# Kernel optimization log

Measured on AMD Instinct MI355X. Metric: run time of the kernel, lower is better.

## Reference

```python
import jax, jax.numpy as jnp
import numpy as np

H = 2048          # hidden_size
I = 8192          # intermediate_size (shared expert)
E = 32            # num_experts
K = 4             # num_experts_per_tok
M = 1408          # moe_intermediate_size
B, S = 2, 1024


def setup_inputs() -> dict:
    key = jax.random.key(0)
    ks = jax.random.split(key, 7)
    scale = 0.02
    return {
        "hidden_states": jax.random.normal(ks[0], (B, S, H), dtype=jnp.float32),
        "gate_w": jax.random.normal(ks[1], (H, E), dtype=jnp.float32) * scale,
        "w1": jax.random.normal(ks[2], (E, H, M), dtype=jnp.float32) * scale,  # expert up-proj
        "w2": jax.random.normal(ks[3], (E, M, H), dtype=jnp.float32) * scale,  # expert down-proj
        "ws1": jax.random.normal(ks[4], (H, I), dtype=jnp.float32) * scale,    # shared up-proj
        "ws2": jax.random.normal(ks[5], (I, H), dtype=jnp.float32) * scale,    # shared down-proj
    }


def reference(hidden_states, gate_w, w1, w2, ws1, ws2):
    b, s, h = hidden_states.shape
    x = hidden_states.reshape(-1, h)                      # [T, H]

    # shared expert: Linear -> SiLU -> Linear
    shared = jax.nn.silu(x @ ws1) @ ws2                   # [T, H]

    # router: top-k logits, softmax over the k selected logits
    router_logits = x @ gate_w                            # [T, E]
    top_vals, top_idx = jax.lax.top_k(router_logits, K)   # [T, K]
    routing_weights = jax.nn.softmax(top_vals, axis=-1)   # [T, K]

    # combine weights: scatter top-k weights into dense [T, E]
    cw = (jax.nn.one_hot(top_idx, E, dtype=x.dtype)
          * routing_weights[..., None]).sum(axis=1)       # [T, E]

    # expert FFNs (dense over experts, weighted combine)
    a = jax.nn.silu(jnp.einsum('th,ehm->tem', x, w1))     # [T, E, M]
    expert_out = jnp.einsum('tem,emh,te->th', a, w2, cw)  # [T, H]

    output = (shared + expert_out).reshape(b, s, h)
    return output, router_logits.reshape(b, s, E)
```

## Files before the change

### kernel.cpp

```cpp
#include <hip/hip_runtime.h>

#define H_ 2048
#define E_ 32
#define KSEL 4
#define M_ 1408
#define I_ 8192
#define T_ 2048

typedef __bf16 bf16;
typedef bf16 bf16x8 __attribute__((ext_vector_type(8)));
typedef float f32x4 __attribute__((ext_vector_type(4)));
typedef unsigned short u16x8 __attribute__((ext_vector_type(8)));
typedef unsigned int u32x4 __attribute__((ext_vector_type(4)));

static __device__ __forceinline__ unsigned short bfb(float f) {
  return __builtin_bit_cast(unsigned short, (bf16)f);
}

static __device__ __forceinline__ void gload_lds16(const void* g, void* l) {
  __builtin_amdgcn_global_load_lds((const __attribute__((address_space(1))) void*)g,
                                   (__attribute__((address_space(3))) void*)l, 16, 0, 0);
}

static __device__ __forceinline__ float silu_f(float v) {
  return v / (1.f + __expf(-v));
}

static __device__ __forceinline__ void wave_argmax(float& v, int& vi) {
  #pragma unroll
  for (int off = 32; off >= 1; off >>= 1) {
    float ov = __shfl_xor(v, off);
    int   oi = __shfl_xor(vi, off);
    if (ov > v || (ov == v && oi < vi)) { v = ov; vi = oi; }
  }
}

__global__ __launch_bounds__(256) void prep_k(float* __restrict__ out, int* __restrict__ counts) {
  size_t i = ((size_t)blockIdx.x * 256 + threadIdx.x) * 4;
  *(float4*)(out + i) = make_float4(0.f, 0.f, 0.f, 0.f);
  if (blockIdx.x == 0 && threadIdx.x < E_) counts[threadIdx.x] = 0;
}

__global__ __launch_bounds__(256) void cvt_k(const float* __restrict__ x, unsigned short* __restrict__ xb) {
  size_t i = ((size_t)blockIdx.x * 256 + threadIdx.x) * 8;
  float4 a = *(const float4*)(x + i);
  float4 b = *(const float4*)(x + i + 4);
  u16x8 o;
  o[0]=bfb(a.x); o[1]=bfb(a.y); o[2]=bfb(a.z); o[3]=bfb(a.w);
  o[4]=bfb(b.x); o[5]=bfb(b.y); o[6]=bfb(b.z); o[7]=bfb(b.w);
  *(u16x8*)(xb + i) = o;
}

__global__ __launch_bounds__(256) void combine_k(const float* __restrict__ sc, float* __restrict__ out) {
  size_t i = ((size_t)blockIdx.x * 256 + threadIdx.x) * 4;
  int t = (int)(i >> 11);
  int h = (int)(i & 2047);
  const float* s = sc + (size_t)(t * 4) * H_ + h;
  float4 a = *(const float4*)(s);
  float4 b = *(const float4*)(s + H_);
  float4 c = *(const float4*)(s + 2 * H_);
  float4 d = *(const float4*)(s + 3 * H_);
  float4 o = *(const float4*)(out + i);
  o.x += a.x + b.x + c.x + d.x;
  o.y += a.y + b.y + c.y + d.y;
  o.z += a.z + b.z + c.z + d.z;
  o.w += a.w + b.w + c.w + d.w;
  *(float4*)(out + i) = o;
}

__global__ __launch_bounds__(64) void router_k(const float* __restrict__ x, const float* __restrict__ gw,
                                               float* __restrict__ logits, int* __restrict__ counts,
                                               int* __restrict__ tlist, float* __restrict__ wlist) {
  int t = blockIdx.x;
  int l = threadIdx.x;
  int e = l & 31;
  int half = l >> 5;
  const float* xr = x + (size_t)t * H_ + half * (H_/2);
  const float* g  = gw + (size_t)(half * (H_/2)) * E_ + e;
  float a0=0.f, a1=0.f, a2=0.f, a3=0.f;
  for (int h = 0; h < H_/2; h += 4) {
    a0 = fmaf(xr[h],   g[(size_t)h*E_],     a0);
    a1 = fmaf(xr[h+1], g[(size_t)(h+1)*E_], a1);
    a2 = fmaf(xr[h+2], g[(size_t)(h+2)*E_], a2);
    a3 = fmaf(xr[h+3], g[(size_t)(h+3)*E_], a3);
  }
  float acc = (a0+a1)+(a2+a3);
  acc += __shfl_xor(acc, 32);
  if (l < E_) logits[(size_t)t*E_ + l] = acc;

  float cur = (l < E_) ? acc : -INFINITY;
  int myidx = (l < E_) ? e : 1000;
  float tv0,tv1,tv2,tv3; int ti0,ti1,ti2,ti3;
  { float v=cur; int vi=myidx; wave_argmax(v,vi); tv0=v; ti0=vi; if (myidx==vi) cur=-INFINITY; }
  { float v=cur; int vi=myidx; wave_argmax(v,vi); tv1=v; ti1=vi; if (myidx==vi) cur=-INFINITY; }
  { float v=cur; int vi=myidx; wave_argmax(v,vi); tv2=v; ti2=vi; if (myidx==vi) cur=-INFINITY; }
  { float v=cur; int vi=myidx; wave_argmax(v,vi); tv3=v; ti3=vi; }
  float w0 = 1.f;
  float w1 = __expf(tv1 - tv0);
  float w2 = __expf(tv2 - tv0);
  float w3 = __expf(tv3 - tv0);
  float inv = 1.f / (w0+w1+w2+w3);
  if (l < KSEL) {
    float myw = ((l==0)?w0:(l==1)?w1:(l==2)?w2:w3) * inv;
    int   myi = ((l==0)?ti0:(l==1)?ti1:(l==2)?ti2:ti3);
    int pos = atomicAdd(&counts[myi], 1);
    tlist[myi*T_ + pos] = (t << 2) | l;
    wlist[myi*T_ + pos] = myw;
  }
}

template<int MODE, int KDIM, int NDIM, int ASTR, int KSPLIT>
__global__ __launch_bounds__(256) void gemm_k(
    const bf16* __restrict__ A, const float* __restrict__ Bf,
    bf16* __restrict__ Cb, float* __restrict__ Cf,
    const int* __restrict__ tlist, const float* __restrict__ wlist,
    const int* __restrict__ counts)
{
  __shared__ __align__(16) char smem[16384];
  char* As = smem;
  char* Bs = smem + 8192;
  const int tid = threadIdx.x;

  int mt, nt, e = 0, kz = 0;
  int nrows = T_;
  const int* lst = nullptr;
  const float* Bp = Bf;
  if constexpr (MODE == 2 || MODE == 3) {
    constexpr int NT = NDIM / 128;
    e  = blockIdx.x / NT;
    nt = blockIdx.x % NT;
    mt = blockIdx.y;
    nrows = counts[e];
    if (mt * 128 >= nrows) return;
    lst = tlist + e*T_;
    Bp = Bf + (size_t)e * ((size_t)KDIM * NDIM);
    if constexpr (KSPLIT > 1) kz = blockIdx.z;
  } else {
    constexpr int NWG = 16 * (NDIM / 128);
    constexpr int CPX = NWG / 8;
    int id = blockIdx.x;
    int lg = (id & 7) * CPX + (id >> 3);
    mt = lg & 15;
    nt = lg >> 4;
    if constexpr (KSPLIT > 1) kz = blockIdx.z;
  }
  const int mrow0 = mt*128, ncol0 = nt*128;

  const bf16* abase[2];
  int aoffs[2];
  #pragma unroll
  for (int hh = 0; hh < 2; ++hh) {
    int lidx = hh*256 + tid;
    int row  = lidx >> 2;
    int slog = (lidx & 3) ^ (row & 3);
    aoffs[hh] = slog * 8;
    int ri = mrow0 + row;
    if constexpr (MODE == 2) {
      int tt = (ri < nrows) ? (lst[ri] >> 2) : 0;
      abase[hh] = A + (size_t)tt * ASTR;
    } else if constexpr (MODE == 3) {
      int ar = (ri < nrows) ? lst[ri] : 0;
      abase[hh] = A + (size_t)ar * ASTR;
    } else {
      abase[hh] = A + (size_t)ri * ASTR;
    }
  }

  const int bn = tid & 127;
  const int bh = tid >> 7;
  const float* bsrc0 = Bp + (size_t)(bh * 16) * NDIM + ncol0 + bn;
  char* bdst0 = Bs + (bh*2)*2048 + bn*16;

  const int l  = tid & 63;
  const int wv = tid >> 6;
  const int wr = wv >> 1, wc = wv & 1;
  const int ss = l >> 4;

  f32x4 acc[4][4] = {};

  constexpr int ITERS = KDIM / 32 / KSPLIT;
  static_assert(ITERS % 2 == 0, "K-loop is 2-unrolled");
  const int kt0 = kz * ITERS;
  const int ktend = kt0 + ITERS;

  float vA0,vA1,vA2,vA3,vA4,vA5,vA6,vA7,vA8,vA9,vA10,vA11,vA12,vA13,vA14,vA15;
  float vB0,vB1,vB2,vB3,vB4,vB5,vB6,vB7,vB8,vB9,vB10,vB11,vB12,vB13,vB14,vB15;

#define LOADB(P, KT) do {                                            \
    const float* bs_ = bsrc0 + (size_t)((KT) * 32) * NDIM;           \
    P##0 = bs_[0];            P##1 = bs_[(size_t)1*NDIM];            \
    P##2 = bs_[(size_t)2*NDIM];  P##3 = bs_[(size_t)3*NDIM];         \
    P##4 = bs_[(size_t)4*NDIM];  P##5 = bs_[(size_t)5*NDIM];         \
    P##6 = bs_[(size_t)6*NDIM];  P##7 = bs_[(size_t)7*NDIM];         \
    P##8 = bs_[(size_t)8*NDIM];  P##9 = bs_[(size_t)9*NDIM];         \
    P##10 = bs_[(size_t)10*NDIM]; P##11 = bs_[(size_t)11*NDIM];      \
    P##12 = bs_[(size_t)12*NDIM]; P##13 = bs_[(size_t)13*NDIM];      \
    P##14 = bs_[(size_t)14*NDIM]; P##15 = bs_[(size_t)15*NDIM];      \
  } while (0)

#define WRITEB(P) do {                                               \
    u32x4 lo_, hi_;                                                  \
    lo_[0] = (unsigned)bfb(P##0)  | ((unsigned)bfb(P##1)  << 16);    \
    lo_[1] = (unsigned)bfb(P##2)  | ((unsigned)bfb(P##3)  << 16);    \
    lo_[2] = (unsigned)bfb(P##4)  | ((unsigned)bfb(P##5)  << 16);    \
    lo_[3] = (unsigned)bfb(P##6)  | ((unsigned)bfb(P##7)  << 16);    \
    hi_[0] = (unsigned)bfb(P##8)  | ((unsigned)bfb(P##9)  << 16);    \
    hi_[1] = (unsigned)bfb(P##10) | ((unsigned)bfb(P##11) << 16);    \
    hi_[2] = (unsigned)bfb(P##12) | ((unsigned)bfb(P##13) << 16);    \
    hi_[3] = (unsigned)bfb(P##14) | ((unsigned)bfb(P##15) << 16);    \
    *(u32x4*)(bdst0)        = lo_;                                   \
    *(u32x4*)(bdst0 + 2048) = hi_;                                   \
  } while (0)

#define MFMA_PHASE(KT) do {                                          \
    bf16x8 af[4], bfr[4];                                            \
    _Pragma("unroll")                                                \
    for (int mf = 0; mf < 4; ++mf) {                                 \
      int r = wr*64 + mf*16 + (l & 15);                              \
      af[mf] = *(const bf16x8*)(As + r*64 + ((ss ^ (r & 3)) << 4));  \
    }                                                                \
    _Pragma("unroll")                                                \
    for (int nf = 0; nf < 4; ++nf) {                                 \
      int c = wc*64 + nf*16 + (l & 15);                              \
      bfr[nf] = *(const bf16x8*)(Bs + ss*2048 + c*16);               \
    }                                                                \
    _Pragma("unroll")                                                \
    for (int mf = 0; mf < 4; ++mf)                                   \
      _Pragma("unroll")                                              \
      for (int nf = 0; nf < 4; ++nf)                                 \
        acc[mf][nf] = __builtin_amdgcn_mfma_f32_16x16x32_bf16(af[mf], bfr[nf], acc[mf][nf], 0, 0, 0); \
  } while (0)

#define ADMA(KT) do {                                                \
    _Pragma("unroll")                                                \
    for (int hh = 0; hh < 2; ++hh)                                   \
      gload_lds16(abase[hh] + (KT)*32 + aoffs[hh], As + (hh*256 + tid)*16); \
  } while (0)

  LOADB(vA, kt0);
  for (int kt = kt0; kt < ktend; kt += 2) {
    __syncthreads();
    ADMA(kt);
    WRITEB(vA);
    __syncthreads();
    LOADB(vB, kt + 1);
    MFMA_PHASE(kt);

    __syncthreads();
    ADMA(kt + 1);
    WRITEB(vB);
    __syncthreads();
    if (kt + 2 < ktend) LOADB(vA, kt + 2);
    MFMA_PHASE(kt + 1);
  }

#undef LOADB
#undef WRITEB
#undef MFMA_PHASE
#undef ADMA

  #pragma unroll
  for (int mf = 0; mf < 4; ++mf) {
    #pragma unroll
    for (int j = 0; j < 4; ++j) {
      const int rloc = wr*64 + mf*16 + (l >> 4)*4 + j;
      const int grow = mrow0 + rloc;
      if constexpr (MODE == 0) {
        #pragma unroll
        for (int nf = 0; nf < 4; ++nf) {
          int col = ncol0 + wc*64 + nf*16 + (l & 15);
          Cb[(size_t)grow * NDIM + col] = (bf16)silu_f(acc[mf][nf][j]);
        }
      } else if constexpr (MODE == 1) {
        #pragma unroll
        for (int nf = 0; nf < 4; ++nf) {
          int col = ncol0 + wc*64 + nf*16 + (l & 15);
          atomicAdd(Cf + (size_t)grow * NDIM + col, acc[mf][nf][j]);
        }
      } else if constexpr (MODE == 2) {
        if (grow < nrows) {
          int entry = lst[grow];
          float wg = wlist[e*T_ + grow];
          #pragma unroll
          for (int nf = 0; nf < 4; ++nf) {
            int col = ncol0 + wc*64 + nf*16 + (l & 15);
            Cb[(size_t)entry * NDIM + col] = (bf16)(silu_f(acc[mf][nf][j]) * wg);
          }
        }
      } else {
        if (grow < nrows) {
          int entry = lst[grow];
          #pragma unroll
          for (int nf = 0; nf < 4; ++nf) {
            int col = ncol0 + wc*64 + nf*16 + (l & 15);
            Cf[(size_t)entry * H_ + col] = acc[mf][nf][j];
          }
        }
      }
    }
  }
}

extern "C" void kernel_launch(void* const* d_in, const int* in_sizes, int n_in,
                              void* d_out, int out_size, void* d_ws, size_t ws_size,
                              hipStream_t stream) {
  const float* x   = (const float*)d_in[0];
  const float* gw  = (const float*)d_in[1];
  const float* w1  = (const float*)d_in[2];
  const float* w2  = (const float*)d_in[3];
  const float* ws1 = (const float*)d_in[4];
  const float* ws2 = (const float*)d_in[5];
  float* out    = (float*)d_out;
  float* logits = out + (size_t)T_ * H_;

  char* ws = (char*)d_ws;
  const size_t off_xb   = 0;
  const size_t off_y1   = off_xb  + (size_t)T_ * H_ * 2;
  const size_t off_act  = off_y1  + (size_t)T_ * I_ * 2;
  const size_t off_cnt  = off_act + (size_t)T_ * 4 * M_ * 2;
  const size_t off_tl   = off_cnt + 256;
  const size_t off_wl   = off_tl  + (size_t)E_ * T_ * 4;
  const size_t off_sc   = off_wl  + (size_t)E_ * T_ * 4;

  const bf16* xb = (const bf16*)(ws + off_xb);
  bf16* y1  = (bf16*)(ws + off_y1);
  bf16* act = (bf16*)(ws + off_act);
  int*  counts = (int*)(ws + off_cnt);
  int*  tlist  = (int*)(ws + off_tl);
  float* wlist = (float*)(ws + off_wl);
  float* scratch = (float*)(ws + off_sc);

  prep_k<<<4096, 256, 0, stream>>>(out, counts);
  router_k<<<T_, 64, 0, stream>>>(x, gw, logits, counts, tlist, wlist);
  cvt_k<<<2048, 256, 0, stream>>>(x, (unsigned short*)(ws + off_xb));

  gemm_k<0, 2048, 8192, 2048, 1><<<dim3(1024), 256, 0, stream>>>(
      xb, ws1, y1, nullptr, nullptr, nullptr, nullptr);
  gemm_k<1, 8192, 2048, 8192, 4><<<dim3(256, 1, 4), 256, 0, stream>>>(
      y1, ws2, nullptr, out, nullptr, nullptr, nullptr);
  gemm_k<2, 2048, 1408, 2048, 1><<<dim3(11*E_, 16), 256, 0, stream>>>(
      xb, w1, act, nullptr, tlist, wlist, counts);
  gemm_k<3, 1408, 2048, 1408, 1><<<dim3(16*E_, 16), 256, 0, stream>>>(
      act, w2, nullptr, scratch, tlist, nullptr, counts);
  combine_k<<<4096, 256, 0, stream>>>(scratch, out);
}
```

Baseline: 827.3 us.

## Use 256-row tiles for expert GEMMs and replace split-K atomics with scratch reduction

The expert GEMM kernels gain a BM template parameter, and the routed expert up- and down-projections now use 256-row M tiles. Each tile reuses its fp32 weight tile, converted to bf16 on the fly, across twice as many tokens, which halves the number of weight reloads per expert. The shared-expert split-K down-projection no longer does atomicAdd into the output. It writes each K-slice to a separate scratch buffer, and combine_k sums these together with the routed-expert partials, so the output zero-fill in prep_k is dropped. In exchange, accumulator registers double for the larger tiles, which may lower occupancy, and combine_k reads an extra 64 MB of scratch.

```diff
diff --git a/kernel.cpp b/kernel.cpp
--- a/kernel.cpp
+++ b/kernel.cpp
@@ -35,10 +35,8 @@
   }
 }
 
-__global__ __launch_bounds__(256) void prep_k(float* __restrict__ out, int* __restrict__ counts) {
-  size_t i = ((size_t)blockIdx.x * 256 + threadIdx.x) * 4;
-  *(float4*)(out + i) = make_float4(0.f, 0.f, 0.f, 0.f);
-  if (blockIdx.x == 0 && threadIdx.x < E_) counts[threadIdx.x] = 0;
+__global__ __launch_bounds__(64) void prep_k(int* __restrict__ counts) {
+  if (threadIdx.x < E_) counts[threadIdx.x] = 0;
 }
 
 __global__ __launch_bounds__(256) void cvt_k(const float* __restrict__ x, unsigned short* __restrict__ xb) {
@@ -51,7 +49,9 @@
   *(u16x8*)(xb + i) = o;
 }
 
-__global__ __launch_bounds__(256) void combine_k(const float* __restrict__ sc, float* __restrict__ out) {
+__global__ __launch_bounds__(256) void combine_k(const float* __restrict__ sc,
+                                                 const float* __restrict__ sc2,
+                                                 float* __restrict__ out) {
   size_t i = ((size_t)blockIdx.x * 256 + threadIdx.x) * 4;
   int t = (int)(i >> 11);
   int h = (int)(i & 2047);
@@ -60,11 +60,16 @@
   float4 b = *(const float4*)(s + H_);
   float4 c = *(const float4*)(s + 2 * H_);
   float4 d = *(const float4*)(s + 3 * H_);
-  float4 o = *(const float4*)(out + i);
-  o.x += a.x + b.x + c.x + d.x;
-  o.y += a.y + b.y + c.y + d.y;
-  o.z += a.z + b.z + c.z + d.z;
-  o.w += a.w + b.w + c.w + d.w;
+  float4 o;
+  o.x = a.x + b.x + c.x + d.x;
+  o.y = a.y + b.y + c.y + d.y;
+  o.z = a.z + b.z + c.z + d.z;
+  o.w = a.w + b.w + c.w + d.w;
+  #pragma unroll
+  for (int kz = 0; kz < 4; ++kz) {
+    float4 v = *(const float4*)(sc2 + (size_t)kz * T_ * H_ + i);
+    o.x += v.x; o.y += v.y; o.z += v.z; o.w += v.w;
+  }
   *(float4*)(out + i) = o;
 }
 
@@ -109,16 +114,18 @@
   }
 }
 
-template<int MODE, int KDIM, int NDIM, int ASTR, int KSPLIT>
+template<int MODE, int KDIM, int NDIM, int ASTR, int KSPLIT, int BM>
 __global__ __launch_bounds__(256) void gemm_k(
     const bf16* __restrict__ A, const float* __restrict__ Bf,
     bf16* __restrict__ Cb, float* __restrict__ Cf,
     const int* __restrict__ tlist, const float* __restrict__ wlist,
     const int* __restrict__ counts)
 {
-  __shared__ __align__(16) char smem[16384];
+  constexpr int MFR = BM / 32;
+  constexpr int ACH = BM / 64;
+  __shared__ __align__(16) char smem[BM * 64 + 8192];
   char* As = smem;
-  char* Bs = smem + 8192;
+  char* Bs = smem + BM * 64;
   const int tid = threadIdx.x;
 
   int mt, nt, e = 0, kz = 0;
@@ -131,10 +138,9 @@
     nt = blockIdx.x % NT;
     mt = blockIdx.y;
     nrows = counts[e];
-    if (mt * 128 >= nrows) return;
+    if (mt * BM >= nrows) return;
     lst = tlist + e*T_;
     Bp = Bf + (size_t)e * ((size_t)KDIM * NDIM);
-    if constexpr (KSPLIT > 1) kz = blockIdx.z;
   } else {
     constexpr int NWG = 16 * (NDIM / 128);
     constexpr int CPX = NWG / 8;
@@ -144,25 +150,25 @@
     nt = lg >> 4;
     if constexpr (KSPLIT > 1) kz = blockIdx.z;
   }
-  const int mrow0 = mt*128, ncol0 = nt*128;
-
-  const bf16* abase[2];
-  int aoffs[2];
+  const int mrow0 = mt*BM, ncol0 = nt*128;
+
+  const bf16* abase[ACH];
+  int aoffs[ACH];
   #pragma unroll
-  for (int hh = 0; hh < 2; ++hh) {
-    int lidx = hh*256 + tid;
+  for (int c = 0; c < ACH; ++c) {
+    int lidx = c*256 + tid;
     int row  = lidx >> 2;
     int slog = (lidx & 3) ^ (row & 3);
-    aoffs[hh] = slog * 8;
+    aoffs[c] = slog * 8;
     int ri = mrow0 + row;
     if constexpr (MODE == 2) {
       int tt = (ri < nrows) ? (lst[ri] >> 2) : 0;
-      abase[hh] = A + (size_t)tt * ASTR;
+      abase[c] = A + (size_t)tt * ASTR;
     } else if constexpr (MODE == 3) {
       int ar = (ri < nrows) ? lst[ri] : 0;
-      abase[hh] = A + (size_t)ar * ASTR;
+      abase[c] = A + (size_t)ar * ASTR;
     } else {
-      abase[hh] = A + (size_t)ri * ASTR;
+      abase[c] = A + (size_t)ri * ASTR;
     }
   }
 
@@ -176,7 +182,7 @@
   const int wr = wv >> 1, wc = wv & 1;
   const int ss = l >> 4;
 
-  f32x4 acc[4][4] = {};
+  f32x4 acc[MFR][4] = {};
 
   constexpr int ITERS = KDIM / 32 / KSPLIT;
   static_assert(ITERS % 2 == 0, "K-loop is 2-unrolled");
@@ -213,10 +219,10 @@
   } while (0)
 
 #define MFMA_PHASE(KT) do {                                          \
-    bf16x8 af[4], bfr[4];                                            \
+    bf16x8 af[MFR], bfr[4];                                          \
     _Pragma("unroll")                                                \
-    for (int mf = 0; mf < 4; ++mf) {                                 \
-      int r = wr*64 + mf*16 + (l & 15);                              \
+    for (int mf = 0; mf < MFR; ++mf) {                               \
+      int r = wr*(BM/2) + mf*16 + (l & 15);                          \
       af[mf] = *(const bf16x8*)(As + r*64 + ((ss ^ (r & 3)) << 4));  \
     }                                                                \
     _Pragma("unroll")                                                \
@@ -225,7 +231,7 @@
       bfr[nf] = *(const bf16x8*)(Bs + ss*2048 + c*16);               \
     }                                                                \
     _Pragma("unroll")                                                \
-    for (int mf = 0; mf < 4; ++mf)                                   \
+    for (int mf = 0; mf < MFR; ++mf)                                 \
       _Pragma("unroll")                                              \
       for (int nf = 0; nf < 4; ++nf)                                 \
         acc[mf][nf] = __builtin_amdgcn_mfma_f32_16x16x32_bf16(af[mf], bfr[nf], acc[mf][nf], 0, 0, 0); \
@@ -233,8 +239,8 @@
 
 #define ADMA(KT) do {                                                \
     _Pragma("unroll")                                                \
-    for (int hh = 0; hh < 2; ++hh)                                   \
-      gload_lds16(abase[hh] + (KT)*32 + aoffs[hh], As + (hh*256 + tid)*16); \
+    for (int c = 0; c < ACH; ++c)                                    \
+      gload_lds16(abase[c] + (KT)*32 + aoffs[c], As + (c*256 + tid)*16); \
   } while (0)
 
   LOADB(vA, kt0);
@@ -260,10 +266,10 @@
 #undef ADMA
 
   #pragma unroll
-  for (int mf = 0; mf < 4; ++mf) {
+  for (int mf = 0; mf < MFR; ++mf) {
     #pragma unroll
     for (int j = 0; j < 4; ++j) {
-      const int rloc = wr*64 + mf*16 + (l >> 4)*4 + j;
+      const int rloc = wr*(BM/2) + mf*16 + (l >> 4)*4 + j;
       const int grow = mrow0 + rloc;
       if constexpr (MODE == 0) {
         #pragma unroll
@@ -272,10 +278,11 @@
           Cb[(size_t)grow * NDIM + col] = (bf16)silu_f(acc[mf][nf][j]);
         }
       } else if constexpr (MODE == 1) {
+        float* dst = Cf + (size_t)kz * T_ * H_;
         #pragma unroll
         for (int nf = 0; nf < 4; ++nf) {
           int col = ncol0 + wc*64 + nf*16 + (l & 15);
-          atomicAdd(Cf + (size_t)grow * NDIM + col, acc[mf][nf][j]);
+          dst[(size_t)grow * NDIM + col] = acc[mf][nf][j];
         }
       } else if constexpr (MODE == 2) {
         if (grow < nrows) {
@@ -321,6 +328,7 @@
   const size_t off_tl   = off_cnt + 256;
   const size_t off_wl   = off_tl  + (size_t)E_ * T_ * 4;
   const size_t off_sc   = off_wl  + (size_t)E_ * T_ * 4;
+  const size_t off_sc2  = off_sc  + (size_t)T_ * 4 * H_ * 4;
 
   const bf16* xb = (const bf16*)(ws + off_xb);
   bf16* y1  = (bf16*)(ws + off_y1);
@@ -328,19 +336,20 @@
   int*  counts = (int*)(ws + off_cnt);
   int*  tlist  = (int*)(ws + off_tl);
   float* wlist = (float*)(ws + off_wl);
-  float* scratch = (float*)(ws + off_sc);
-
-  prep_k<<<4096, 256, 0, stream>>>(out, counts);
+  float* scratch  = (float*)(ws + off_sc);
+  float* scratch2 = (float*)(ws + off_sc2);
+
+  prep_k<<<1, 64, 0, stream>>>(counts);
   router_k<<<T_, 64, 0, stream>>>(x, gw, logits, counts, tlist, wlist);
   cvt_k<<<2048, 256, 0, stream>>>(x, (unsigned short*)(ws + off_xb));
 
-  gemm_k<0, 2048, 8192, 2048, 1><<<dim3(1024), 256, 0, stream>>>(
+  gemm_k<0, 2048, 8192, 2048, 1, 128><<<dim3(1024), 256, 0, stream>>>(
       xb, ws1, y1, nullptr, nullptr, nullptr, nullptr);
-  gemm_k<1, 8192, 2048, 8192, 4><<<dim3(256, 1, 4), 256, 0, stream>>>(
-      y1, ws2, nullptr, out, nullptr, nullptr, nullptr);
-  gemm_k<2, 2048, 1408, 2048, 1><<<dim3(11*E_, 16), 256, 0, stream>>>(
+  gemm_k<1, 8192, 2048, 8192, 4, 128><<<dim3(256, 1, 4), 256, 0, stream>>>(
+      y1, ws2, nullptr, scratch2, nullptr, nullptr, nullptr);
+  gemm_k<2, 2048, 1408, 2048, 1, 256><<<dim3(11*E_, 8), 256, 0, stream>>>(
       xb, w1, act, nullptr, tlist, wlist, counts);
-  gemm_k<3, 1408, 2048, 1408, 1><<<dim3(16*E_, 16), 256, 0, stream>>>(
+  gemm_k<3, 1408, 2048, 1408, 1, 256><<<dim3(16*E_, 8), 256, 0, stream>>>(
       act, w2, nullptr, scratch, tlist, nullptr, counts);
-  combine_k<<<4096, 256, 0, stream>>>(scratch, out);
-}
+  combine_k<<<4096, 256, 0, stream>>>(scratch, scratch2, out);
+}
```

Result: slower. 949.5 us (+14.8%).

## Replace split-K atomics with per-split scratch and remap expert GEMM tiles

Applied to the files above, without the earlier changes.

The shared down-projection now writes each K-split's partial result to its own fp32 scratch slice instead of using atomicAdd into the output. The combine kernel sums those four slices together with the expert partials, so the large output-zeroing pass in prep_k is dropped. The expert GEMMs also get a new block-index mapping that interleaves pairs of M tiles per expert and spreads neighbouring blocks across XCD groups. This removes atomic contention and a memset, at the cost of 64MB of extra scratch traffic in combine.

```diff
diff --git a/kernel.cpp b/kernel.cpp
--- a/kernel.cpp
+++ b/kernel.cpp
@@ -35,10 +35,8 @@
   }
 }
 
-__global__ __launch_bounds__(256) void prep_k(float* __restrict__ out, int* __restrict__ counts) {
-  size_t i = ((size_t)blockIdx.x * 256 + threadIdx.x) * 4;
-  *(float4*)(out + i) = make_float4(0.f, 0.f, 0.f, 0.f);
-  if (blockIdx.x == 0 && threadIdx.x < E_) counts[threadIdx.x] = 0;
+__global__ __launch_bounds__(64) void prep_k(int* __restrict__ counts) {
+  if (threadIdx.x < E_) counts[threadIdx.x] = 0;
 }
 
 __global__ __launch_bounds__(256) void cvt_k(const float* __restrict__ x, unsigned short* __restrict__ xb) {
@@ -51,7 +49,9 @@
   *(u16x8*)(xb + i) = o;
 }
 
-__global__ __launch_bounds__(256) void combine_k(const float* __restrict__ sc, float* __restrict__ out) {
+__global__ __launch_bounds__(256) void combine_k(const float* __restrict__ sc,
+                                                 const float* __restrict__ sc2,
+                                                 float* __restrict__ out) {
   size_t i = ((size_t)blockIdx.x * 256 + threadIdx.x) * 4;
   int t = (int)(i >> 11);
   int h = (int)(i & 2047);
@@ -60,11 +60,16 @@
   float4 b = *(const float4*)(s + H_);
   float4 c = *(const float4*)(s + 2 * H_);
   float4 d = *(const float4*)(s + 3 * H_);
-  float4 o = *(const float4*)(out + i);
-  o.x += a.x + b.x + c.x + d.x;
-  o.y += a.y + b.y + c.y + d.y;
-  o.z += a.z + b.z + c.z + d.z;
-  o.w += a.w + b.w + c.w + d.w;
+  float4 o;
+  o.x = a.x + b.x + c.x + d.x;
+  o.y = a.y + b.y + c.y + d.y;
+  o.z = a.z + b.z + c.z + d.z;
+  o.w = a.w + b.w + c.w + d.w;
+  #pragma unroll
+  for (int kz = 0; kz < 4; ++kz) {
+    float4 v = *(const float4*)(sc2 + (size_t)kz * T_ * H_ + i);
+    o.x += v.x; o.y += v.y; o.z += v.z; o.w += v.w;
+  }
   *(float4*)(out + i) = o;
 }
 
@@ -127,14 +132,19 @@
   const float* Bp = Bf;
   if constexpr (MODE == 2 || MODE == 3) {
     constexpr int NT = NDIM / 128;
-    e  = blockIdx.x / NT;
-    nt = blockIdx.x % NT;
-    mt = blockIdx.y;
+    constexpr int NWG = NT * E_ * 2;
+    constexpr int CPX = NWG / 8;
+    int id = blockIdx.x;
+    int lg = (id & 7) * CPX + (id >> 3);
+    int bit = lg & 1;
+    int en  = lg >> 1;
+    e  = en / NT;
+    nt = en % NT;
+    mt = (blockIdx.y == 0) ? bit : (2 + 2*((int)blockIdx.y - 1) + bit);
     nrows = counts[e];
     if (mt * 128 >= nrows) return;
     lst = tlist + e*T_;
     Bp = Bf + (size_t)e * ((size_t)KDIM * NDIM);
-    if constexpr (KSPLIT > 1) kz = blockIdx.z;
   } else {
     constexpr int NWG = 16 * (NDIM / 128);
     constexpr int CPX = NWG / 8;
@@ -272,10 +282,11 @@
           Cb[(size_t)grow * NDIM + col] = (bf16)silu_f(acc[mf][nf][j]);
         }
       } else if constexpr (MODE == 1) {
+        float* dst = Cf + (size_t)kz * T_ * H_;
         #pragma unroll
         for (int nf = 0; nf < 4; ++nf) {
           int col = ncol0 + wc*64 + nf*16 + (l & 15);
-          atomicAdd(Cf + (size_t)grow * NDIM + col, acc[mf][nf][j]);
+          dst[(size_t)grow * NDIM + col] = acc[mf][nf][j];
         }
       } else if constexpr (MODE == 2) {
         if (grow < nrows) {
@@ -321,6 +332,7 @@
   const size_t off_tl   = off_cnt + 256;
   const size_t off_wl   = off_tl  + (size_t)E_ * T_ * 4;
   const size_t off_sc   = off_wl  + (size_t)E_ * T_ * 4;
+  const size_t off_sc2  = off_sc  + (size_t)T_ * 4 * H_ * 4;
 
   const bf16* xb = (const bf16*)(ws + off_xb);
   bf16* y1  = (bf16*)(ws + off_y1);
@@ -328,19 +340,20 @@
   int*  counts = (int*)(ws + off_cnt);
   int*  tlist  = (int*)(ws + off_tl);
   float* wlist = (float*)(ws + off_wl);
-  float* scratch = (float*)(ws + off_sc);
-
-  prep_k<<<4096, 256, 0, stream>>>(out, counts);
+  float* scratch  = (float*)(ws + off_sc);
+  float* scratch2 = (float*)(ws + off_sc2);
+
+  prep_k<<<1, 64, 0, stream>>>(counts);
   router_k<<<T_, 64, 0, stream>>>(x, gw, logits, counts, tlist, wlist);
   cvt_k<<<2048, 256, 0, stream>>>(x, (unsigned short*)(ws + off_xb));
 
   gemm_k<0, 2048, 8192, 2048, 1><<<dim3(1024), 256, 0, stream>>>(
       xb, ws1, y1, nullptr, nullptr, nullptr, nullptr);
   gemm_k<1, 8192, 2048, 8192, 4><<<dim3(256, 1, 4), 256, 0, stream>>>(
-      y1, ws2, nullptr, out, nullptr, nullptr, nullptr);
-  gemm_k<2, 2048, 1408, 2048, 1><<<dim3(11*E_, 16), 256, 0, stream>>>(
+      y1, ws2, nullptr, scratch2, nullptr, nullptr, nullptr);
+  gemm_k<2, 2048, 1408, 2048, 1><<<dim3(11*E_*2, 8), 256, 0, stream>>>(
       xb, w1, act, nullptr, tlist, wlist, counts);
-  gemm_k<3, 1408, 2048, 1408, 1><<<dim3(16*E_, 16), 256, 0, stream>>>(
+  gemm_k<3, 1408, 2048, 1408, 1><<<dim3(16*E_*2, 8), 256, 0, stream>>>(
       act, w2, nullptr, scratch, tlist, nullptr, counts);
-  combine_k<<<4096, 256, 0, stream>>>(scratch, out);
-}
+  combine_k<<<4096, 256, 0, stream>>>(scratch, scratch2, out);
+}
```

Result: no change. 830.4 us (+0.4%).
